# Optimization experiments

Hardware: AMD Instinct MI355X
Metric: run time of the kernel (lower is better)

## Reference

```python
import jax, jax.numpy as jnp
import numpy as np

IMG = 128      # raster_settings.image_size
FOCAL = 1.5    # simple pinhole projection (camera transform)
EPS = 1e-8
B, V, F = 4, 600, 1000


def setup_inputs() -> dict:
    key = jax.random.key(0)
    k1, k2 = jax.random.split(key)
    u = jax.random.uniform(k1, (B, V, 3), dtype=jnp.float32)
    xy = u[..., :2] * 2.0 - 1.0          # x,y in [-1, 1]
    z = u[..., 2:3] * 2.0 + 1.0          # z in [1, 3] (in front of camera)
    verts = jnp.concatenate([xy, z], axis=-1)   # [B, V, 3] world coords
    faces = jax.random.randint(k2, (F, 3), 0, V)  # [F, 3] vertex indices
    return {"verts": verts, "faces": faces}


def _pix_grid(H, W):
    # PyTorch3D NDC convention: +X left, +Y up; pixel centers at (2i+1)/S - 1 flipped.
    xs = 1.0 - (2.0 * jnp.arange(W, dtype=jnp.float32) + 1.0) / W
    ys = 1.0 - (2.0 * jnp.arange(H, dtype=jnp.float32) + 1.0) / H
    px = jnp.broadcast_to(xs[None, :], (H, W)).reshape(-1)  # [P]
    py = jnp.broadcast_to(ys[:, None], (H, W)).reshape(-1)  # [P]
    return px, py


def _edge(ax, ay, bx, by, px, py):
    # signed (twice-)area of triangle (a, b, p)
    return (bx - ax) * (py - ay) - (by - ay) * (px - ax)


def _seg_dist2(px, py, ax, ay, bx, by):
    # squared distance from point p to segment (a, b); all args broadcastable
    ex, ey = bx - ax, by - ay
    dx, dy = px - ax, py - ay
    ee = jnp.maximum(ex * ex + ey * ey, EPS)
    t = jnp.clip((dx * ex + dy * ey) / ee, 0.0, 1.0)
    rx = dx - t * ex
    ry = dy - t * ey
    return rx * rx + ry * ry


def _rasterize_one(v_ndc, faces, H, W):
    fv = v_ndc[faces]                       # [F, 3, 3] face vertices (ndc x, y, view z)
    v0, v1, v2 = fv[:, 0], fv[:, 1], fv[:, 2]
    px, py = _pix_grid(H, W)                # [P], P = H*W
    pxr, pyr = px[None, :], py[None, :]
    # signed face area [F]
    area = _edge(v0[:, 0], v0[:, 1], v1[:, 0], v1[:, 1], v2[:, 0], v2[:, 1])
    # edge functions at every pixel -> unnormalized barycentrics [F, P]
    w0 = _edge(v1[:, 0:1], v1[:, 1:2], v2[:, 0:1], v2[:, 1:2], pxr, pyr)
    w1 = _edge(v2[:, 0:1], v2[:, 1:2], v0[:, 0:1], v0[:, 1:2], pxr, pyr)
    w2 = _edge(v0[:, 0:1], v0[:, 1:2], v1[:, 0:1], v1[:, 1:2], pxr, pyr)
    denom = jnp.where(jnp.abs(area) > EPS, area, EPS)[:, None]
    s0, s1, s2 = w0 / denom, w1 / denom, w2 / denom
    zpix = s0 * v0[:, 2:3] + s1 * v1[:, 2:3] + s2 * v2[:, 2:3]  # [F, P]
    inside = (s0 >= 0) & (s1 >= 0) & (s2 >= 0) \
             & (jnp.abs(area)[:, None] > EPS) & (zpix > 0)
    zcand = jnp.where(inside, zpix, jnp.inf)
    idx = jnp.argmin(zcand, axis=0)                       # [P] winning face per pixel
    gather = lambda a: jnp.take_along_axis(a, idx[None, :], axis=0)[0]
    zmin = gather(zcand)
    hit = jnp.isfinite(zmin)
    b0, b1, b2 = gather(s0), gather(s1), gather(s2)       # winner barycentrics [P]
    # signed squared point-triangle distance at the winning face (negative inside)
    fw = fv[idx]                                          # [P, 3, 3]
    a, b, c = fw[:, 0], fw[:, 1], fw[:, 2]
    d2 = jnp.minimum(
        jnp.minimum(_seg_dist2(px, py, a[:, 0], a[:, 1], b[:, 0], b[:, 1]),
                    _seg_dist2(px, py, b[:, 0], b[:, 1], c[:, 0], c[:, 1])),
        _seg_dist2(px, py, c[:, 0], c[:, 1], a[:, 0], a[:, 1]))
    pix_to_face = jnp.where(hit, idx, -1).reshape(H, W)
    zbuf = jnp.where(hit, zmin, -1.0).reshape(H, W)
    bary = jnp.where(hit[:, None], jnp.stack([b0, b1, b2], -1), -1.0).reshape(H, W, 3)
    dists = jnp.where(hit, -d2, -1.0).reshape(H, W)
    return pix_to_face, zbuf, bary, dists


def reference(verts, faces):
    # camera transform: identity world-to-view, perspective projection, keep view z
    x = FOCAL * verts[..., 0] / verts[..., 2]
    y = FOCAL * verts[..., 1] / verts[..., 2]
    v_ndc = jnp.stack([x, y, verts[..., 2]], axis=-1)     # [B, V, 3]
    rast = lambda v: _rasterize_one(v, faces, IMG, IMG)
    pix_to_face, zbuf, bary, dists = jax.vmap(rast)(v_ndc)
    return pix_to_face, zbuf, bary, dists
```

## Files before the change

### kernel.cpp

```cpp
#include <hip/hip_runtime.h>
#include <math.h>

namespace {

constexpr int IMG  = 128;
constexpr int NPIX = IMG * IMG;
constexpr int B    = 4;
constexpr int V    = 600;
constexpr int F    = 1000;
constexpr float FOCALF = 1.5f;
constexpr float EPSF   = 1e-8f;
constexpr float SLACK  = 1e-5f;
constexpr float ZEPS    = 1e-4f;
constexpr float DENSAFE = 1e-3f;

__device__ inline float seg_dist2(float px, float py, float ax, float ay,
                                  float bx, float by) {
#pragma clang fp contract(off)
    float ex = bx - ax, ey = by - ay;
    float dx = px - ax, dy = py - ay;
    float ee = fmaxf(ex * ex + ey * ey, EPSF);
    float t  = (dx * ex + dy * ey) / ee;
    t = fminf(fmaxf(t, 0.0f), 1.0f);
    float rx = dx - t * ex;
    float ry = dy - t * ey;
    return rx * rx + ry * ry;
}

__global__ __launch_bounds__(256) void setup_clear(const float* __restrict__ verts,
                                                   const int* __restrict__ faces,
                                                   float* __restrict__ fdata,
                                                   unsigned long long* __restrict__ zbest) {
#pragma clang fp contract(off)
    int t = blockIdx.x * 256 + threadIdx.x;
    zbest[t] = ~0ULL;
    if (t >= B * F) return;
    int b = t / F, f = t - b * F;
    int i0 = faces[f * 3 + 0], i1 = faces[f * 3 + 1], i2 = faces[f * 3 + 2];
    const float* vb = verts + (size_t)b * V * 3;
    float x0 = vb[i0 * 3], y0 = vb[i0 * 3 + 1], z0 = vb[i0 * 3 + 2];
    float x1 = vb[i1 * 3], y1 = vb[i1 * 3 + 1], z1 = vb[i1 * 3 + 2];
    float x2 = vb[i2 * 3], y2 = vb[i2 * 3 + 1], z2 = vb[i2 * 3 + 2];
    float ax = (FOCALF * x0) / z0, ay = (FOCALF * y0) / z0;
    float bx = (FOCALF * x1) / z1, by = (FOCALF * y1) / z1;
    float cx = (FOCALF * x2) / z2, cy = (FOCALF * y2) / z2;
    float e0x = cx - bx, e0y = cy - by;
    float e1x = ax - cx, e1y = ay - cy;
    float e2x = bx - ax, e2y = by - ay;
    float den = e2x * (cy - ay) - e2y * (cx - ax);
    if (!(fabsf(den) > EPSF)) den = 0.0f;
    const float rd = __builtin_amdgcn_rcpf(den);
    float* o = fdata + (size_t)t * 20;
    o[0]  = e0x;  o[1]  = e0y;  o[2]  = bx;       o[3]  = by;
    o[4]  = e1x;  o[5]  = e1y;  o[6]  = cx;       o[7]  = cy;
    o[8]  = e2x;  o[9]  = e2y;  o[10] = ax;       o[11] = ay;
    o[12] = den;  o[13] = z0 * rd; o[14] = z1 * rd; o[15] = z2 * rd;
    o[16] = z0;   o[17] = z1;   o[18] = z2;       o[19] = 0.0f;
}

__global__ __launch_bounds__(512, 8) void rast(const float* __restrict__ fdata,
                                               unsigned long long* __restrict__ zbest) {
#pragma clang fp contract(off)
    __shared__ float4 sface[64 * 5];
    __shared__ unsigned int lticket;
    const int tid  = threadIdx.x;
    const int lane = tid & 63;
    const int bk   = blockIdx.x;
    const int ch   = bk & 15;
    const int b    = (bk >> 4) & 3;
    const int slice = bk >> 6;
    if (tid == 0) lticket = 0u;

    const int f0 = ch * 64;
    const int sz = min(64, F - f0);
    const int fl = min(f0 + lane, F - 1);
    const float4* fd4 = (const float4*)(fdata + ((size_t)b * F + fl) * 20);
    const float4 q0 = fd4[0], q1 = fd4[1], q2 = fd4[2], q3 = fd4[3], q4 = fd4[4];
    if (tid < 64) {
        sface[tid * 5 + 0] = q0;
        sface[tid * 5 + 1] = q1;
        sface[tid * 5 + 2] = q2;
        sface[tid * 5 + 3] = q3;
        sface[tid * 5 + 4] = q4;
    }
    __syncthreads();

    const bool valid = (lane < sz) & (q3.x != 0.0f);
    const float s = q3.x > 0.0f ? 1.0f : -1.0f;
    const float g0x = s * q0.x, g0y = s * q0.y;
    const float g1x = s * q1.x, g1y = s * q1.y;
    const float g2x = s * q2.x, g2y = s * q2.y;
    const bool c0y = g0x >= 0.0f, c0x = g0y >= 0.0f;
    const bool c1y = g1x >= 0.0f, c1x = g1y >= 0.0f;
    const bool c2y = g2x >= 0.0f, c2x = g2y >= 0.0f;

    const int dpx = lane & 7, dpy = lane >> 3;

    for (;;) {
        unsigned int j = 0;
        if (lane == 0) j = atomicAdd(&lticket, 1u);
        j = (unsigned int)__shfl((int)j, 0);
        if (j >= 16u) break;
        const unsigned int jj = (j + (unsigned int)ch) & 15u;

        const int row = (slice >> 2) + 4 * (int)(jj >> 2);
        const int col = (slice & 3) + 4 * (int)(jj & 3);
        const int ix0 = col * 8, iy0 = row * 8;
        const int ix  = ix0 + dpx, iy = iy0 + dpy;
        const float px = 1.0f - (2.0f * (float)ix + 1.0f) / (float)IMG;
        const float py = 1.0f - (2.0f * (float)iy + 1.0f) / (float)IMG;
        const float pxmax = 1.0f - (2.0f * (float)ix0 + 1.0f) / (float)IMG;
        const float pxmin = 1.0f - (2.0f * (float)(ix0 + 7) + 1.0f) / (float)IMG;
        const float pymax = 1.0f - (2.0f * (float)iy0 + 1.0f) / (float)IMG;
        const float pymin = 1.0f - (2.0f * (float)(iy0 + 7) + 1.0f) / (float)IMG;

        const int gp = b * NPIX + iy * IMG + ix;
        const unsigned ztop = (unsigned)(zbest[gp] >> 32);
        float zbf  = (ztop == 0xFFFFFFFFu) ? INFINITY : __uint_as_float(ztop);
        float zbfp = zbf + ZEPS;

        bool pass = valid;
        pass &= (g0x * ((c0y ? pymax : pymin) - q0.w)
               - g0y * ((c0x ? pxmin : pxmax) - q0.z)) >= -SLACK;
        pass &= (g1x * ((c1y ? pymax : pymin) - q1.w)
               - g1y * ((c1x ? pxmin : pxmax) - q1.z)) >= -SLACK;
        pass &= (g2x * ((c2y ? pymax : pymin) - q2.w)
               - g2y * ((c2x ? pxmin : pxmax) - q2.z)) >= -SLACK;

        unsigned long long pmin = ~0ULL;
        unsigned long long mask = __ballot(pass);
        while (mask) {
            const int sl = __builtin_ctzll(mask);
            mask &= mask - 1;
            const float4 r0 = sface[sl * 5 + 0];
            const float4 r1 = sface[sl * 5 + 1];
            const float4 r2 = sface[sl * 5 + 2];
            const float4 r3 = sface[sl * 5 + 3];
            const float den = r3.x;
            float w0 = r0.x * (py - r0.w) - r0.y * (px - r0.z);
            float w1 = r1.x * (py - r1.w) - r1.y * (px - r1.z);
            float w2 = r2.x * (py - r2.w) - r2.y * (px - r2.z);

            const bool insd = !(w0 * den < 0.0f) & !(w1 * den < 0.0f) &
                              !(w2 * den < 0.0f);
            if (!__any(insd)) continue;

            const float zt = w0 * r3.y + w1 * r3.z + w2 * r3.w;
            const bool densmall = fabsf(den) < DENSAFE;
            const bool need = insd & (densmall | ((zt < zbfp) & (zt > -ZEPS)));
            if (__any(need)) {
                const unsigned ds = __float_as_uint(den) >> 31;
                const bool in0 = (w0 == 0.0f) | ((__float_as_uint(w0) >> 31) == ds);
                const bool in1 = (w1 == 0.0f) | ((__float_as_uint(w1) >> 31) == ds);
                const bool in2 = (w2 == 0.0f) | ((__float_as_uint(w2) >> 31) == ds);
                if (in0 & in1 & in2) {
                    const float4 r4 = sface[sl * 5 + 4];
                    float s0 = w0 / den, s1 = w1 / den, s2 = w2 / den;
                    float z  = s0 * r4.x + s1 * r4.y + s2 * r4.z;
                    if (z > 0.0f) {
                        unsigned long long pk =
                            ((unsigned long long)__float_as_uint(z) << 32) |
                            (unsigned)(f0 + sl);
                        pmin = pmin < pk ? pmin : pk;
                        zbf  = fminf(zbf, z);
                        zbfp = zbf + ZEPS;
                    }
                }
            }
        }
        if (pmin != ~0ULL) atomicMin(&zbest[gp], pmin);
    }
}

__global__ __launch_bounds__(256) void pass2(const float* __restrict__ fdata,
                                             const unsigned long long* __restrict__ zbest,
                                             float* __restrict__ out) {
#pragma clang fp contract(off)
    const int gp = blockIdx.x * 256 + threadIdx.x;
    const int b  = gp >> 14;
    const int p  = gp & (NPIX - 1);
    const int ix = p & (IMG - 1), iy = p >> 7;

    unsigned long long packed = zbest[gp];
    float o_face = -1.0f, o_z = -1.0f, o_b0 = -1.0f, o_b1 = -1.0f,
          o_b2 = -1.0f, o_d = -1.0f;

    if (packed != ~0ULL) {
        const int   idx = (int)(unsigned)(packed & 0xffffffffu);
        const float z   = __uint_as_float((unsigned)(packed >> 32));
        const float px  = 1.0f - (2.0f * (float)ix + 1.0f) / (float)IMG;
        const float py  = 1.0f - (2.0f * (float)iy + 1.0f) / (float)IMG;

        const float4* fd4 = (const float4*)(fdata + ((size_t)b * F + idx) * 20);
        float4 q0 = fd4[0], q1 = fd4[1], q2 = fd4[2], q3 = fd4[3], q4 = fd4[4];
        float den = q3.x;
        float w0 = q0.x * (py - q0.w) - q0.y * (px - q0.z);
        float w1 = q1.x * (py - q1.w) - q1.y * (px - q1.z);
        float w2 = q2.x * (py - q2.w) - q2.y * (px - q2.z);
        float s0 = w0 / den, s1 = w1 / den, s2 = w2 / den;
        (void)q4;

        float d2 = fminf(fminf(seg_dist2(px, py, q2.z, q2.w, q0.z, q0.w),
                               seg_dist2(px, py, q0.z, q0.w, q1.z, q1.w)),
                         seg_dist2(px, py, q1.z, q1.w, q2.z, q2.w));
        o_face = (float)idx; o_z = z;
        o_b0 = s0; o_b1 = s1; o_b2 = s2;
        o_d = -d2;
    }

    out[gp]            = o_face;
    out[B * NPIX + gp] = o_z;
    const int bary_base = 2 * B * NPIX;
    out[bary_base + gp * 3 + 0] = o_b0;
    out[bary_base + gp * 3 + 1] = o_b1;
    out[bary_base + gp * 3 + 2] = o_b2;
    out[5 * B * NPIX + gp] = o_d;
}

}

extern "C" void kernel_launch(void* const* d_in, const int* in_sizes, int n_in,
                              void* d_out, int out_size, void* d_ws, size_t ws_size,
                              hipStream_t stream) {
    const float* verts = (const float*)d_in[0];
    const int*   faces = (const int*)d_in[1];
    float* out = (float*)d_out;

    char* ws = (char*)d_ws;
    unsigned long long* zbest = (unsigned long long*)ws;
    float* fdata = (float*)(ws + (size_t)B * NPIX * 8);

    setup_clear<<<B * NPIX / 256, 256, 0, stream>>>(verts, faces, fdata, zbest);
    rast<<<1024, 512, 0, stream>>>(fdata, zbest);
    pass2<<<B * NPIX / 256, 256, 0, stream>>>(fdata, zbest, out);
}
```

Before: 31.80 us.

## Sort faces by min depth and skip chunks occluded by current zbuffer

```diff
diff --git a/kernel.cpp b/kernel.cpp
--- a/kernel.cpp
+++ b/kernel.cpp
@@ -8,11 +8,40 @@
 constexpr int B    = 4;
 constexpr int V    = 600;
 constexpr int F    = 1000;
+constexpr int FP   = 1024;
 constexpr float FOCALF = 1.5f;
 constexpr float EPSF   = 1e-8f;
 constexpr float SLACK  = 1e-5f;
 constexpr float ZEPS    = 1e-4f;
 constexpr float DENSAFE = 1e-3f;
+constexpr float ZMARGIN = 0.03f;
+
+struct FaceRec {
+    float e0x, e0y, bx, by;
+    float e1x, e1y, cx, cy;
+    float e2x, e2y, ax, ay;
+    float den, z0, z1, z2;
+};
+
+__device__ inline FaceRec project_face(const float* __restrict__ vb,
+                                       const int* __restrict__ faces, int f) {
+#pragma clang fp contract(off)
+    FaceRec r;
+    int i0 = faces[f * 3 + 0], i1 = faces[f * 3 + 1], i2 = faces[f * 3 + 2];
+    float x0 = vb[i0 * 3], y0 = vb[i0 * 3 + 1]; r.z0 = vb[i0 * 3 + 2];
+    float x1 = vb[i1 * 3], y1 = vb[i1 * 3 + 1]; r.z1 = vb[i1 * 3 + 2];
+    float x2 = vb[i2 * 3], y2 = vb[i2 * 3 + 1]; r.z2 = vb[i2 * 3 + 2];
+    r.ax = (FOCALF * x0) / r.z0; r.ay = (FOCALF * y0) / r.z0;
+    r.bx = (FOCALF * x1) / r.z1; r.by = (FOCALF * y1) / r.z1;
+    r.cx = (FOCALF * x2) / r.z2; r.cy = (FOCALF * y2) / r.z2;
+    r.e0x = r.cx - r.bx; r.e0y = r.cy - r.by;
+    r.e1x = r.ax - r.cx; r.e1y = r.ay - r.cy;
+    r.e2x = r.bx - r.ax; r.e2y = r.by - r.ay;
+    float den = r.e2x * (r.cy - r.ay) - r.e2y * (r.cx - r.ax);
+    if (!(fabsf(den) > EPSF)) den = 0.0f;
+    r.den = den;
+    return r;
+}
 
 __device__ inline float seg_dist2(float px, float py, float ax, float ay,
                                   float bx, float by) {
@@ -27,41 +56,88 @@
     return rx * rx + ry * ry;
 }
 
-__global__ __launch_bounds__(256) void setup_clear(const float* __restrict__ verts,
-                                                   const int* __restrict__ faces,
-                                                   float* __restrict__ fdata,
-                                                   unsigned long long* __restrict__ zbest) {
-#pragma clang fp contract(off)
-    int t = blockIdx.x * 256 + threadIdx.x;
-    zbest[t] = ~0ULL;
-    if (t >= B * F) return;
-    int b = t / F, f = t - b * F;
-    int i0 = faces[f * 3 + 0], i1 = faces[f * 3 + 1], i2 = faces[f * 3 + 2];
+__global__ __launch_bounds__(1024) void prep(const float* __restrict__ verts,
+                                             const int* __restrict__ faces,
+                                             float* __restrict__ fdata,
+                                             int* __restrict__ rank,
+                                             unsigned long long* __restrict__ zbest) {
+#pragma clang fp contract(off)
+    __shared__ int   hist[64];
+    __shared__ int   sortedid[FP];
+    __shared__ float stmp[FP];
+    const int tid = threadIdx.x;
+    const int b   = blockIdx.x;
     const float* vb = verts + (size_t)b * V * 3;
-    float x0 = vb[i0 * 3], y0 = vb[i0 * 3 + 1], z0 = vb[i0 * 3 + 2];
-    float x1 = vb[i1 * 3], y1 = vb[i1 * 3 + 1], z1 = vb[i1 * 3 + 2];
-    float x2 = vb[i2 * 3], y2 = vb[i2 * 3 + 1], z2 = vb[i2 * 3 + 2];
-    float ax = (FOCALF * x0) / z0, ay = (FOCALF * y0) / z0;
-    float bx = (FOCALF * x1) / z1, by = (FOCALF * y1) / z1;
-    float cx = (FOCALF * x2) / z2, cy = (FOCALF * y2) / z2;
-    float e0x = cx - bx, e0y = cy - by;
-    float e1x = ax - cx, e1y = ay - cy;
-    float e2x = bx - ax, e2y = by - ay;
-    float den = e2x * (cy - ay) - e2y * (cx - ax);
-    if (!(fabsf(den) > EPSF)) den = 0.0f;
-    const float rd = __builtin_amdgcn_rcpf(den);
-    float* o = fdata + (size_t)t * 20;
-    o[0]  = e0x;  o[1]  = e0y;  o[2]  = bx;       o[3]  = by;
-    o[4]  = e1x;  o[5]  = e1y;  o[6]  = cx;       o[7]  = cy;
-    o[8]  = e2x;  o[9]  = e2y;  o[10] = ax;       o[11] = ay;
-    o[12] = den;  o[13] = z0 * rd; o[14] = z1 * rd; o[15] = z2 * rd;
-    o[16] = z0;   o[17] = z1;   o[18] = z2;       o[19] = 0.0f;
+
+    for (int i = tid; i < NPIX; i += FP) zbest[b * NPIX + i] = ~0ULL;
+
+    if (tid < 64) hist[tid] = 0;
+    sortedid[tid] = -1;
+    __syncthreads();
+
+    int mybucket = -1;
+    if (tid < F) {
+        FaceRec r = project_face(vb, faces, tid);
+        if (r.den != 0.0f) {
+            float minz = fminf(fminf(r.z0, r.z1), r.z2);
+            mybucket = min(63, max(0, (int)((minz - 1.0f) * 32.0f)));
+            atomicAdd(&hist[mybucket], 1);
+        }
+    }
+    __syncthreads();
+    if (tid == 0) {
+        int acc = 0;
+        for (int i = 0; i < 64; ++i) { int h = hist[i]; hist[i] = acc; acc += h; }
+    }
+    __syncthreads();
+    if (mybucket >= 0) {
+        int pos = atomicAdd(&hist[mybucket], 1);
+        sortedid[pos] = tid;
+    }
+    __syncthreads();
+
+    const int id   = sortedid[tid];
+    const bool real = (id >= 0);
+    FaceRec r = {};
+    float azr = 0.0f, bzr = 0.0f, czr = 0.0f;
+    float tsk = INFINITY;
+    bool sliver = false;
+    if (real) {
+        r = project_face(vb, faces, id);
+        const float rd = __builtin_amdgcn_rcpf(r.den);
+        azr = r.z0 * rd; bzr = r.z1 * rd; czr = r.z2 * rd;
+        float minz = fminf(fminf(r.z0, r.z1), r.z2);
+        sliver = fabsf(r.den) < DENSAFE;
+        if (!sliver) tsk = minz - fmaxf(ZMARGIN, 0.011f * minz);
+    }
+    stmp[tid] = tsk;
+    __syncthreads();
+    float v = stmp[tid];
+    for (int off = 1; off < FP; off <<= 1) {
+        float o = (tid + off < FP) ? stmp[tid + off] : INFINITY;
+        __syncthreads();
+        v = fminf(v, o);
+        stmp[tid] = v;
+        __syncthreads();
+    }
+
+    float* o = fdata + (size_t)(b * FP + tid) * 24;
+    o[0]  = r.e0x; o[1]  = r.e0y; o[2]  = r.bx;  o[3]  = r.by;
+    o[4]  = r.e1x; o[5]  = r.e1y; o[6]  = r.cx;  o[7]  = r.cy;
+    o[8]  = r.e2x; o[9]  = r.e2y; o[10] = r.ax;  o[11] = r.ay;
+    o[12] = r.den; o[13] = azr;   o[14] = bzr;   o[15] = czr;
+    o[16] = r.z0;  o[17] = r.z1;  o[18] = r.z2;
+    o[19] = __int_as_float(real ? id : 0);
+    o[20] = v;
+    o[21] = sliver ? 1.0f : 0.0f;
+    o[22] = 0.0f; o[23] = 0.0f;
+    if (real) rank[b * F + id] = tid;
 }
 
 __global__ __launch_bounds__(512, 8) void rast(const float* __restrict__ fdata,
                                                unsigned long long* __restrict__ zbest) {
 #pragma clang fp contract(off)
-    __shared__ float4 sface[64 * 5];
+    __shared__ float4 sface[64 * 6];
     __shared__ unsigned int lticket;
     const int tid  = threadIdx.x;
     const int lane = tid & 63;
@@ -72,20 +148,19 @@
     if (tid == 0) lticket = 0u;
 
     const int f0 = ch * 64;
-    const int sz = min(64, F - f0);
-    const int fl = min(f0 + lane, F - 1);
-    const float4* fd4 = (const float4*)(fdata + ((size_t)b * F + fl) * 20);
-    const float4 q0 = fd4[0], q1 = fd4[1], q2 = fd4[2], q3 = fd4[3], q4 = fd4[4];
+    const float4* fd4 = (const float4*)(fdata + (size_t)(b * FP + f0 + lane) * 24);
+    const float4 q0 = fd4[0], q1 = fd4[1], q2 = fd4[2], q3 = fd4[3],
+                 q4 = fd4[4], q5 = fd4[5];
     if (tid < 64) {
-        sface[tid * 5 + 0] = q0;
-        sface[tid * 5 + 1] = q1;
-        sface[tid * 5 + 2] = q2;
-        sface[tid * 5 + 3] = q3;
-        sface[tid * 5 + 4] = q4;
-    }
-    __syncthreads();
-
-    const bool valid = (lane < sz) & (q3.x != 0.0f);
+        sface[tid * 6 + 0] = q0; sface[tid * 6 + 1] = q1;
+        sface[tid * 6 + 2] = q2; sface[tid * 6 + 3] = q3;
+        sface[tid * 6 + 4] = q4; sface[tid * 6 + 5] = q5;
+    }
+    const unsigned long long slivmask = __ballot(q5.y != 0.0f);
+    __syncthreads();
+    const float minskip = sface[5].x;
+
+    const bool valid = (q3.x != 0.0f);
     const float s = q3.x > 0.0f ? 1.0f : -1.0f;
     const float g0x = s * q0.x, g0y = s * q0.y;
     const float g1x = s * q1.x, g1y = s * q1.y;
@@ -119,6 +194,9 @@
         float zbf  = (ztop == 0xFFFFFFFFu) ? INFINITY : __uint_as_float(ztop);
         float zbfp = zbf + ZEPS;
 
+        const bool itemdead = __all(minskip > zbf);
+        if (itemdead & (slivmask == 0ULL)) continue;
+
         bool pass = valid;
         pass &= (g0x * ((c0y ? pymax : pymin) - q0.w)
                - g0y * ((c0x ? pxmin : pxmax) - q0.z)) >= -SLACK;
@@ -129,13 +207,25 @@
 
         unsigned long long pmin = ~0ULL;
         unsigned long long mask = __ballot(pass);
+        bool checks = true;
+        if (itemdead) { mask &= slivmask; checks = false; }
+
         while (mask) {
             const int sl = __builtin_ctzll(mask);
+            const unsigned long long bit = mask & (unsigned long long)(-(long long)mask);
             mask &= mask - 1;
-            const float4 r0 = sface[sl * 5 + 0];
-            const float4 r1 = sface[sl * 5 + 1];
-            const float4 r2 = sface[sl * 5 + 2];
-            const float4 r3 = sface[sl * 5 + 3];
+            if (checks) {
+                const float suffm = sface[sl * 6 + 5].x;
+                if (__all(suffm > zbf)) {
+                    mask = (mask | bit) & slivmask;
+                    checks = false;
+                    continue;
+                }
+            }
+            const float4 r0 = sface[sl * 6 + 0];
+            const float4 r1 = sface[sl * 6 + 1];
+            const float4 r2 = sface[sl * 6 + 2];
+            const float4 r3 = sface[sl * 6 + 3];
             const float den = r3.x;
             float w0 = r0.x * (py - r0.w) - r0.y * (px - r0.z);
             float w1 = r1.x * (py - r1.w) - r1.y * (px - r1.z);
@@ -154,13 +244,13 @@
                 const bool in1 = (w1 == 0.0f) | ((__float_as_uint(w1) >> 31) == ds);
                 const bool in2 = (w2 == 0.0f) | ((__float_as_uint(w2) >> 31) == ds);
                 if (in0 & in1 & in2) {
-                    const float4 r4 = sface[sl * 5 + 4];
+                    const float4 r4 = sface[sl * 6 + 4];
                     float s0 = w0 / den, s1 = w1 / den, s2 = w2 / den;
                     float z  = s0 * r4.x + s1 * r4.y + s2 * r4.z;
                     if (z > 0.0f) {
+                        const unsigned fj = __float_as_uint(r4.w);
                         unsigned long long pk =
-                            ((unsigned long long)__float_as_uint(z) << 32) |
-                            (unsigned)(f0 + sl);
+                            ((unsigned long long)__float_as_uint(z) << 32) | fj;
                         pmin = pmin < pk ? pmin : pk;
                         zbf  = fminf(zbf, z);
                         zbfp = zbf + ZEPS;
@@ -173,6 +263,7 @@
 }
 
 __global__ __launch_bounds__(256) void pass2(const float* __restrict__ fdata,
+                                             const int* __restrict__ rank,
                                              const unsigned long long* __restrict__ zbest,
                                              float* __restrict__ out) {
 #pragma clang fp contract(off)
@@ -191,14 +282,14 @@
         const float px  = 1.0f - (2.0f * (float)ix + 1.0f) / (float)IMG;
         const float py  = 1.0f - (2.0f * (float)iy + 1.0f) / (float)IMG;
 
-        const float4* fd4 = (const float4*)(fdata + ((size_t)b * F + idx) * 20);
-        float4 q0 = fd4[0], q1 = fd4[1], q2 = fd4[2], q3 = fd4[3], q4 = fd4[4];
+        const int pos = rank[b * F + idx];
+        const float4* fd4 = (const float4*)(fdata + (size_t)(b * FP + pos) * 24);
+        float4 q0 = fd4[0], q1 = fd4[1], q2 = fd4[2], q3 = fd4[3];
         float den = q3.x;
         float w0 = q0.x * (py - q0.w) - q0.y * (px - q0.z);
         float w1 = q1.x * (py - q1.w) - q1.y * (px - q1.z);
         float w2 = q2.x * (py - q2.w) - q2.y * (px - q2.z);
         float s0 = w0 / den, s1 = w1 / den, s2 = w2 / den;
-        (void)q4;
 
         float d2 = fminf(fminf(seg_dist2(px, py, q2.z, q2.w, q0.z, q0.w),
                                seg_dist2(px, py, q0.z, q0.w, q1.z, q1.w)),
@@ -229,8 +320,9 @@
     char* ws = (char*)d_ws;
     unsigned long long* zbest = (unsigned long long*)ws;
     float* fdata = (float*)(ws + (size_t)B * NPIX * 8);
-
-    setup_clear<<<B * NPIX / 256, 256, 0, stream>>>(verts, faces, fdata, zbest);
+    int*   rank  = (int*)(ws + (size_t)B * NPIX * 8 + (size_t)B * FP * 96);
+
+    prep<<<B, 1024, 0, stream>>>(verts, faces, fdata, rank, zbest);
     rast<<<1024, 512, 0, stream>>>(fdata, zbest);
-    pass2<<<B * NPIX / 256, 256, 0, stream>>>(fdata, zbest, out);
-}
+    pass2<<<B * NPIX / 256, 256, 0, stream>>>(fdata, rank, zbest, out);
+}
```

Result: slower. 40.90 us (+28.6%).
